# Kernel optimization log

Hardware: AMD Instinct MI355X
Metric: run time of the kernel (lower is better)

The kernel has to match this reference:

```python
import jax, jax.numpy as jnp
import numpy as np

N_GENOMES = 30000
N_GENES = 240000
N_SAMPLES = 128
N_SEQS = 80000


def setup_inputs() -> dict:
    key = jax.random.key(0)
    k0, k1, k2, k3, k4 = jax.random.split(key, 5)
    A = jax.random.normal(k0, (N_GENOMES, N_SAMPLES), dtype=jnp.float32)  # log-abundance
    B = jax.random.normal(k1, (N_GENOMES, N_SAMPLES), dtype=jnp.float32)  # log-PTR
    pos = jax.random.uniform(k2, (N_GENES,), dtype=jnp.float32)           # dist from ori, in [0,1)
    genome_idx = jnp.sort(jax.random.randint(k3, (N_GENES,), 0, N_GENOMES))  # block one-hot of `members`
    seq_idx = jax.random.randint(k4, (N_GENES,), 0, N_SEQS)               # gene -> md5 sequence map
    return {"A": A, "B": B, "pos": pos, "genome_idx": genome_idx, "seq_idx": seq_idx}


def reference(A, B, pos, genome_idx, seq_idx):
    # G = members @ A + 1 - dists @ B, where members/dists are one-hot per gene row
    # -> gather rows of A and B by genome assignment, scale B row by gene position.
    G = A[genome_idx] + 1.0 - pos[:, None] * B[genome_idx]   # (m, s)
    # gene_to_seq @ exp(G) -> segment sum of exp(G) over gene->sequence assignment
    return jax.ops.segment_sum(jnp.exp(G), seq_idx, num_segments=N_SEQS)  # (k, s)
```

## Files before the change

kernel.cpp:

```cpp
#include <hip/hip_runtime.h>
#include <hip/hip_fp16.h>

#define N_GENOMES 30000
#define N_GENES   240000
#define N_SAMPLES 128
#define N_SEQS    80000
#define CAP       32

#define SCATTER_BLOCKS  ((N_GENES + 255) / 256)
#define COMPRESS_BLOCKS ((N_GENOMES * 32) / 256)

typedef float        f32x4 __attribute__((ext_vector_type(4)));
typedef unsigned int u32x4 __attribute__((ext_vector_type(4)));

#define LOG2E 1.4426950408889634f

#if __has_builtin(__builtin_amdgcn_exp2f)
#define EXP2F(x) __builtin_amdgcn_exp2f(x)
#else
#define EXP2F(x) exp2f(x)
#endif

__global__ __launch_bounds__(256) void prep_kernel(
    const float* __restrict__ A,
    const float* __restrict__ B,
    const float* __restrict__ pos,
    const int*   __restrict__ genome_idx,
    const int*   __restrict__ seq_idx,
    int*          __restrict__ cnt,
    unsigned int* __restrict__ bucket,
    float4*       __restrict__ AB16)
{
    int b = blockIdx.x;
    if (b < SCATTER_BLOCKS) {
        int gene = b * 256 + threadIdx.x;
        if (gene >= N_GENES) return;
        int   s = seq_idx[gene];
        int   g = genome_idx[gene];
        float p = pos[gene];
        unsigned int q   = (unsigned int)(p * 131072.0f);
        unsigned int rec = (unsigned int)g | (q << 15);
        int slot = atomicAdd(&cnt[s], 1);
        if (slot < CAP) bucket[s * CAP + slot] = rec;
    } else {
        int idx = (b - SCATTER_BLOCKS) * 256 + threadIdx.x;
        f32x4 a  = __builtin_nontemporal_load((const f32x4*)A + idx);
        f32x4 bb = __builtin_nontemporal_load((const f32x4*)B + idx);
        __half2 h[4];
        h[0] = __floats2half2_rn((a.x + 1.0f) * LOG2E, (a.y + 1.0f) * LOG2E);
        h[1] = __floats2half2_rn((a.z + 1.0f) * LOG2E, (a.w + 1.0f) * LOG2E);
        h[2] = __floats2half2_rn(bb.x * LOG2E, bb.y * LOG2E);
        h[3] = __floats2half2_rn(bb.z * LOG2E, bb.w * LOG2E);
        AB16[idx] = *reinterpret_cast<float4*>(h);
    }
}

__global__ __launch_bounds__(256) void accum_kernel(
    const float4*       __restrict__ AB16,
    const int*          __restrict__ cnt,
    const unsigned int* __restrict__ bucket,
    float*              __restrict__ out)
{
    int idx  = blockIdx.x * blockDim.x + threadIdx.x;
    int seq  = idx >> 5;
    int quad = idx & 31;
    if (seq >= N_SEQS) return;

    const u32x4* bk4 = reinterpret_cast<const u32x4*>(bucket + seq * CAP);
    u32x4 r4 = bk4[0];
    int   n  = cnt[seq];
    if (n > CAP) n = CAP;

    float4 acc = make_float4(0.f, 0.f, 0.f, 0.f);

    {
        unsigned int r[4] = { r4.x, r4.y, r4.z, r4.w };
        float4 raw[4];
        #pragma unroll
        for (int j = 0; j < 4; ++j) {
            unsigned int g = (j < n) ? (r[j] & 0x7fffu) : 0u;
            raw[j] = AB16[g * 32 + quad];
        }
        #pragma unroll
        for (int j = 0; j < 4; ++j) {
            float p = (float)(r[j] >> 15) * (1.0f / 131072.0f);
            const __half2* hp = reinterpret_cast<const __half2*>(&raw[j]);
            float2 a01 = __half22float2(hp[0]);
            float2 a23 = __half22float2(hp[1]);
            float2 b01 = __half22float2(hp[2]);
            float2 b23 = __half22float2(hp[3]);
            if (j < n) {
                acc.x += EXP2F(a01.x - p * b01.x);
                acc.y += EXP2F(a01.y - p * b01.y);
                acc.z += EXP2F(a23.x - p * b23.x);
                acc.w += EXP2F(a23.y - p * b23.y);
            }
        }
    }

    if (n > 4) {
        for (int i0 = 4; i0 < n; i0 += 4) {
            u32x4 t4 = bk4[i0 >> 2];
            unsigned int r[4] = { t4.x, t4.y, t4.z, t4.w };
            float4 raw[4];
            #pragma unroll
            for (int j = 0; j < 4; ++j) {
                unsigned int g = (i0 + j < n) ? (r[j] & 0x7fffu) : 0u;
                raw[j] = AB16[g * 32 + quad];
            }
            #pragma unroll
            for (int j = 0; j < 4; ++j) {
                float p = (float)(r[j] >> 15) * (1.0f / 131072.0f);
                const __half2* hp = reinterpret_cast<const __half2*>(&raw[j]);
                float2 a01 = __half22float2(hp[0]);
                float2 a23 = __half22float2(hp[1]);
                float2 b01 = __half22float2(hp[2]);
                float2 b23 = __half22float2(hp[3]);
                if (i0 + j < n) {
                    acc.x += EXP2F(a01.x - p * b01.x);
                    acc.y += EXP2F(a01.y - p * b01.y);
                    acc.z += EXP2F(a23.x - p * b23.x);
                    acc.w += EXP2F(a23.y - p * b23.y);
                }
            }
        }
    }

    f32x4 o = { acc.x, acc.y, acc.z, acc.w };
    __builtin_nontemporal_store(o, (f32x4*)out + seq * 32 + quad);
}

extern "C" void kernel_launch(void* const* d_in, const int* in_sizes, int n_in,
                              void* d_out, int out_size, void* d_ws, size_t ws_size,
                              hipStream_t stream) {
    const float* A    = (const float*)d_in[0];
    const float* B    = (const float*)d_in[1];
    const float* pos  = (const float*)d_in[2];
    const int*   gidx = (const int*)d_in[3];
    const int*   sidx = (const int*)d_in[4];
    float*       out  = (float*)d_out;

    char*         ws     = (char*)d_ws;
    float4*       AB16   = (float4*)ws;
    int*          cnt    = (int*)(ws + (size_t)N_GENOMES * 32 * 16);
    unsigned int* bucket = (unsigned int*)(cnt + N_SEQS);

    hipMemsetAsync(cnt, 0, N_SEQS * sizeof(int), stream);

    prep_kernel<<<SCATTER_BLOCKS + COMPRESS_BLOCKS, 256, 0, stream>>>(
        A, B, pos, gidx, sidx, cnt, bucket, AB16);

    const int total = N_SEQS * 32;
    accum_kernel<<<total / 256, 256, 0, stream>>>(
        AB16, cnt, bucket, out);
}
```

Baseline: 125.1 us.

## Split AB16 table into sample-group slabs and separate first-four bucket slots

The packed half-precision genome table is rearranged into 8 slabs, one per group of 16 samples, and each accumulation block now handles a single slab for 64 sequences. The goal is a smaller working set per block, so random genome gathers hit in L2/MALL more often. The bucket array is also split into a dense first-4 slot array plus an overflow area, which makes the common-case bucket reads contiguous. In exchange, each sequence's bucket and count are read 8 times (once per slab), and output writes become strided across blocks.

```diff
diff --git a/kernel.cpp b/kernel.cpp
--- a/kernel.cpp
+++ b/kernel.cpp
@@ -28,7 +28,8 @@
     const int*   __restrict__ genome_idx,
     const int*   __restrict__ seq_idx,
     int*          __restrict__ cnt,
-    unsigned int* __restrict__ bucket,
+    unsigned int* __restrict__ bucket0,
+    unsigned int* __restrict__ bucketOv,
     float4*       __restrict__ AB16)
 {
     int b = blockIdx.x;
@@ -41,7 +42,8 @@
         unsigned int q   = (unsigned int)(p * 131072.0f);
         unsigned int rec = (unsigned int)g | (q << 15);
         int slot = atomicAdd(&cnt[s], 1);
-        if (slot < CAP) bucket[s * CAP + slot] = rec;
+        if (slot < 4)        bucket0[s * 4 + slot] = rec;
+        else if (slot < CAP) bucketOv[s * 28 + (slot - 4)] = rec;
     } else {
         int idx = (b - SCATTER_BLOCKS) * 256 + threadIdx.x;
         f32x4 a  = __builtin_nontemporal_load((const f32x4*)A + idx);
@@ -51,25 +53,32 @@
         h[1] = __floats2half2_rn((a.z + 1.0f) * LOG2E, (a.w + 1.0f) * LOG2E);
         h[2] = __floats2half2_rn(bb.x * LOG2E, bb.y * LOG2E);
         h[3] = __floats2half2_rn(bb.z * LOG2E, bb.w * LOG2E);
-        AB16[idx] = *reinterpret_cast<float4*>(h);
+        int genome = idx >> 5;
+        int quad   = idx & 31;
+        int qg = quad >> 2, qw = quad & 3;
+        AB16[((size_t)qg * N_GENOMES + genome) * 4 + qw] =
+            *reinterpret_cast<float4*>(h);
     }
 }
 
 __global__ __launch_bounds__(256) void accum_kernel(
     const float4*       __restrict__ AB16,
     const int*          __restrict__ cnt,
-    const unsigned int* __restrict__ bucket,
+    const unsigned int* __restrict__ bucket0,
+    const unsigned int* __restrict__ bucketOv,
     float*              __restrict__ out)
 {
-    int idx  = blockIdx.x * blockDim.x + threadIdx.x;
-    int seq  = idx >> 5;
-    int quad = idx & 31;
-    if (seq >= N_SEQS) return;
+    int b   = blockIdx.x;
+    int qg  = b & 7;
+    int tid = threadIdx.x;
+    int seq = (b >> 3) * 64 + (tid >> 2);
+    int qw  = tid & 3;
 
-    const u32x4* bk4 = reinterpret_cast<const u32x4*>(bucket + seq * CAP);
-    u32x4 r4 = bk4[0];
+    u32x4 r4 = reinterpret_cast<const u32x4*>(bucket0)[seq];
     int   n  = cnt[seq];
     if (n > CAP) n = CAP;
+
+    const float4* T = AB16 + (size_t)qg * N_GENOMES * 4 + qw;
 
     float4 acc = make_float4(0.f, 0.f, 0.f, 0.f);
 
@@ -79,7 +88,7 @@
         #pragma unroll
         for (int j = 0; j < 4; ++j) {
             unsigned int g = (j < n) ? (r[j] & 0x7fffu) : 0u;
-            raw[j] = AB16[g * 32 + quad];
+            raw[j] = T[(size_t)g * 4];
         }
         #pragma unroll
         for (int j = 0; j < 4; ++j) {
@@ -99,14 +108,16 @@
     }
 
     if (n > 4) {
+        const u32x4* bkv =
+            reinterpret_cast<const u32x4*>(bucketOv + (size_t)seq * 28);
         for (int i0 = 4; i0 < n; i0 += 4) {
-            u32x4 t4 = bk4[i0 >> 2];
+            u32x4 t4 = bkv[(i0 - 4) >> 2];
             unsigned int r[4] = { t4.x, t4.y, t4.z, t4.w };
             float4 raw[4];
             #pragma unroll
             for (int j = 0; j < 4; ++j) {
                 unsigned int g = (i0 + j < n) ? (r[j] & 0x7fffu) : 0u;
-                raw[j] = AB16[g * 32 + quad];
+                raw[j] = T[(size_t)g * 4];
             }
             #pragma unroll
             for (int j = 0; j < 4; ++j) {
@@ -126,8 +137,9 @@
         }
     }
 
+    int quad = (qg << 2) + qw;
     f32x4 o = { acc.x, acc.y, acc.z, acc.w };
-    __builtin_nontemporal_store(o, (f32x4*)out + seq * 32 + quad);
+    __builtin_nontemporal_store(o, (f32x4*)out + (size_t)seq * 32 + quad);
 }
 
 extern "C" void kernel_launch(void* const* d_in, const int* in_sizes, int n_in,
@@ -140,17 +152,17 @@
     const int*   sidx = (const int*)d_in[4];
     float*       out  = (float*)d_out;
 
-    char*         ws     = (char*)d_ws;
-    float4*       AB16   = (float4*)ws;
-    int*          cnt    = (int*)(ws + (size_t)N_GENOMES * 32 * 16);
-    unsigned int* bucket = (unsigned int*)(cnt + N_SEQS);
+    char*         ws       = (char*)d_ws;
+    float4*       AB16     = (float4*)ws;
+    int*          cnt      = (int*)(ws + (size_t)N_GENOMES * 32 * 16);
+    unsigned int* bucket0  = (unsigned int*)(cnt + N_SEQS);
+    unsigned int* bucketOv = bucket0 + (size_t)N_SEQS * 4;
 
     hipMemsetAsync(cnt, 0, N_SEQS * sizeof(int), stream);
 
     prep_kernel<<<SCATTER_BLOCKS + COMPRESS_BLOCKS, 256, 0, stream>>>(
-        A, B, pos, gidx, sidx, cnt, bucket, AB16);
+        A, B, pos, gidx, sidx, cnt, bucket0, bucketOv, AB16);
 
-    const int total = N_SEQS * 32;
-    accum_kernel<<<total / 256, 256, 0, stream>>>(
-        AB16, cnt, bucket, out);
+    accum_kernel<<<(N_SEQS / 64) * 8, 256, 0, stream>>>(
+        AB16, cnt, bucket0, bucketOv, out);
 }
```

New measurement: 122.5 us. 1.02x faster.
